# Optimization experiments

Hardware: AMD Instinct MI355X
Metric: run time of the kernel (lower is better)

The kernel has to match this reference:

```python
import jax, jax.numpy as jnp
import numpy as np

N = 100000      # nodes
E = 600000      # edges per relation (avg degree 6 per relation here per edge list)
R = 3           # num_relations
D_IN = 128
D_OUT = 128


def setup_inputs() -> dict:
    key = jax.random.key(0)
    ks = jax.random.split(key, 7)
    x = jax.random.normal(ks[0], (N, D_IN), dtype=jnp.float32)
    src = jax.random.randint(ks[1], (R, E), 0, N, dtype=jnp.int32)   # column indices of sparse adj
    dst = jax.random.randint(ks[2], (R, E), 0, N, dtype=jnp.int32)   # row indices of sparse adj
    vals = jax.random.uniform(ks[3], (R, E), dtype=jnp.float32)      # nonzero values
    scale = 1.0 / np.sqrt(D_IN)
    W_self = jax.random.normal(ks[4], (D_OUT, D_IN), dtype=jnp.float32) * scale
    b_self = jnp.zeros((D_OUT,), dtype=jnp.float32)
    W_rels = jax.random.normal(ks[5], (R, D_OUT, D_IN), dtype=jnp.float32) * scale
    return {"x": x, "src": src, "dst": dst, "vals": vals,
            "W_self": W_self, "b_self": b_self, "W_rels": W_rels}


def reference(x, src, dst, vals, W_self, b_self, W_rels):
    # self-loop: Linear(in_dim, out_dim) with bias
    out = x @ W_self.T + b_self                               # [N, D_OUT]
    n = x.shape[0]
    for r in range(R):
        # sparse.mm(adj_r, x): row i gets sum_j adj[i,j] * x[j]
        msg = vals[r][:, None] * x[src[r]]                    # [E, D_IN] gather
        agg = jax.ops.segment_sum(msg, dst[r], num_segments=n)  # [N, D_IN] scatter-add
        out = out + agg @ W_rels[r].T                         # per-relation Linear (no bias)
    return out
```

## Files before the change

kernel.cpp:

```cpp
#include <hip/hip_runtime.h>


typedef __attribute__((ext_vector_type(8))) short bf16x8;
typedef __attribute__((ext_vector_type(4))) float f32x4;
typedef unsigned short u16;

__device__ inline void split2(float v, u16& h, u16& l) {
  unsigned u = __float_as_uint(v);
  u16 hu = (u16)(u >> 16);
  float r = v - __uint_as_float((unsigned)hu << 16);
  unsigned ur = __float_as_uint(r);
  l = (u16)((ur + 0x7FFF + ((ur >> 16) & 1)) >> 16);
  h = hu;
}


__global__ void hist_kernel(const int* __restrict__ dst, int* __restrict__ cursor,
                            int total, int N, int E) {
  int i = blockIdx.x * 256 + threadIdx.x;
  if (i >= total) return;
  int r = i / E;
  atomicAdd(&cursor[r * N + dst[i]], 1);
}

__global__ __launch_bounds__(256)
void scanA_kernel(const int* __restrict__ cursor, int* __restrict__ blockSums, int keys) {
  int t = threadIdx.x;
  int idx = blockIdx.x * 1024 + t * 4;
  int s = 0;
  if (idx < keys) {
    int4 v = *(const int4*)(cursor + idx);
    s = v.x + v.y + v.z + v.w;
  }
  __shared__ int lds[256];
  lds[t] = s;
  __syncthreads();
  for (int off = 128; off > 0; off >>= 1) {
    if (t < off) lds[t] += lds[t + off];
    __syncthreads();
  }
  if (t == 0) blockSums[blockIdx.x] = lds[0];
}

__global__ __launch_bounds__(1024)
void scanB_kernel(int* __restrict__ blockSums, int nb) {
  __shared__ int lds[1024];
  int t = threadIdx.x;
  int v0 = (t < nb) ? blockSums[t] : 0;
  lds[t] = v0;
  __syncthreads();
  for (int off = 1; off < 1024; off <<= 1) {
    int v = (t >= off) ? lds[t - off] : 0;
    __syncthreads();
    lds[t] += v;
    __syncthreads();
  }
  if (t < nb) blockSums[t] = lds[t] - v0;
}

__global__ __launch_bounds__(256)
void scanC_kernel(int* __restrict__ cursor, const int* __restrict__ blockSums, int keys) {
  int t = threadIdx.x;
  int idx = blockIdx.x * 1024 + t * 4;
  int4 v = make_int4(0, 0, 0, 0);
  if (idx < keys) v = *(const int4*)(cursor + idx);
  int s = v.x + v.y + v.z + v.w;
  __shared__ int lds[256];
  lds[t] = s;
  __syncthreads();
  for (int off = 1; off < 256; off <<= 1) {
    int u = (t >= off) ? lds[t - off] : 0;
    __syncthreads();
    lds[t] += u;
    __syncthreads();
  }
  int run = blockSums[blockIdx.x] + lds[t] - s;
  if (idx < keys) {
    int4 o;
    o.x = run;              run += v.x;
    o.y = run;              run += v.y;
    o.z = run;              run += v.z;
    o.w = run;
    *(int4*)(cursor + idx) = o;
  }
}

__global__ void fill_kernel(const int* __restrict__ dst, const int* __restrict__ src,
                            const float* __restrict__ vals, int* __restrict__ cursor,
                            int2* __restrict__ edges, int total, int N, int E) {
  int i = blockIdx.x * 256 + threadIdx.x;
  if (i >= total) return;
  int r = i / E;
  int key = r * N + dst[i];
  int p = atomicAdd(&cursor[key], 1);
  edges[p] = make_int2(src[i], __float_as_int(vals[i]));
}


__global__ __launch_bounds__(256)
void aggregate_kernel(const float* __restrict__ x, const int2* __restrict__ edges,
                      const int* __restrict__ cursor, float* __restrict__ Agg,
                      int N, int R, int keys) {
  int wid = blockIdx.x * 4 + (threadIdx.x >> 6);
  if (wid >= keys) return;
  int lane = threadIdx.x & 63;
  int r = (wid < N) ? 0 : ((wid < 2 * N) ? 1 : 2);
  int d = wid - r * N;
  int pstart = (wid == 0) ? 0 : cursor[wid - 1];
  int pend   = cursor[wid];
  float2 acc = {0.f, 0.f};
  int p = pstart;
  for (; p + 4 <= pend; p += 4) {
    int2 e0 = edges[p + 0];
    int2 e1 = edges[p + 1];
    int2 e2 = edges[p + 2];
    int2 e3 = edges[p + 3];
    float2 x0 = *(const float2*)(x + (size_t)e0.x * 128 + lane * 2);
    float2 x1 = *(const float2*)(x + (size_t)e1.x * 128 + lane * 2);
    float2 x2 = *(const float2*)(x + (size_t)e2.x * 128 + lane * 2);
    float2 x3 = *(const float2*)(x + (size_t)e3.x * 128 + lane * 2);
    float v0 = __int_as_float(e0.y), v1 = __int_as_float(e1.y);
    float v2 = __int_as_float(e2.y), v3 = __int_as_float(e3.y);
    acc.x += v0 * x0.x; acc.y += v0 * x0.y;
    acc.x += v1 * x1.x; acc.y += v1 * x1.y;
    acc.x += v2 * x2.x; acc.y += v2 * x2.y;
    acc.x += v3 * x3.x; acc.y += v3 * x3.y;
  }
  for (; p < pend; ++p) {
    int2 e = edges[p];
    float2 xv = *(const float2*)(x + (size_t)e.x * 128 + lane * 2);
    float v = __int_as_float(e.y);
    acc.x += v * xv.x; acc.y += v * xv.y;
  }
  *(float2*)(Agg + (size_t)d * (R * 128) + r * 128 + lane * 2) = acc;
}


__global__ __launch_bounds__(256)
void split_w_kernel(const float* __restrict__ Wself, const float* __restrict__ Wrels,
                    u16* __restrict__ Whi, u16* __restrict__ Wlo) {
  int e = (blockIdx.x * 256 + threadIdx.x) * 4;
  if (e >= 128 * 512) return;
  int n = e >> 9;
  int k = e & 511;
  #pragma unroll
  for (int j = 0; j < 4; ++j) {
    int kk = k + j;
    float v;
    if (kk < 128) v = Wself[n * 128 + kk];
    else {
      int q = (kk - 128) >> 7;
      v = Wrels[q * 16384 + n * 128 + ((kk - 128) & 127)];
    }
    u16 h, l;
    split2(v, h, l);
    Whi[n * 512 + kk] = h;
    Wlo[n * 512 + kk] = l;
  }
}


__global__ __launch_bounds__(256)
void gemm_mfma(const float* __restrict__ x, const float* __restrict__ Agg,
               const u16* __restrict__ Whi, const u16* __restrict__ Wlo,
               const float* __restrict__ bias, float* __restrict__ out, int N) {
  __shared__ __align__(16) u16 Ah[128][40];
  __shared__ __align__(16) u16 Al[128][40];
  __shared__ __align__(16) u16 Bh[128][40];
  __shared__ __align__(16) u16 Bl[128][40];

  const int m0   = blockIdx.x * 128;
  const int t    = threadIdx.x;
  const int lane = t & 63;
  const int wave = t >> 6;
  const int wm   = wave >> 1;
  const int wn   = wave & 1;
  const int lr   = lane & 15;
  const int kg   = lane >> 4;

  f32x4 acc[4][4];
  #pragma unroll
  for (int i = 0; i < 4; ++i)
    #pragma unroll
    for (int j = 0; j < 4; ++j)
      #pragma unroll
      for (int c = 0; c < 4; ++c) acc[i][j][c] = 0.f;

  for (int ph = 0; ph < 16; ++ph) {
    __syncthreads();
    #pragma unroll
    for (int i = 0; i < 4; ++i) {
      int L   = t + i * 256;
      int row = L >> 3;
      int c4  = L & 7;
      int gm  = m0 + row;
      float4 v = make_float4(0.f, 0.f, 0.f, 0.f);
      if (gm < N) {
        const float* Ap = (ph < 4) ? (x + (size_t)gm * 128 + ph * 32)
                                   : (Agg + (size_t)gm * 384 + (ph - 4) * 32);
        v = *(const float4*)(Ap + c4 * 4);
      }
      ushort4 h4, l4;
      split2(v.x, h4.x, l4.x);
      split2(v.y, h4.y, l4.y);
      split2(v.z, h4.z, l4.z);
      split2(v.w, h4.w, l4.w);
      *(ushort4*)&Ah[row][c4 * 4] = h4;
      *(ushort4*)&Al[row][c4 * 4] = l4;
    }
    #pragma unroll
    for (int i = 0; i < 4; ++i) {
      int L   = t + i * 256;
      int row = L >> 3;
      int c4  = L & 7;
      *(ushort4*)&Bh[row][c4 * 4] = *(const ushort4*)(Whi + row * 512 + ph * 32 + c4 * 4);
      *(ushort4*)&Bl[row][c4 * 4] = *(const ushort4*)(Wlo + row * 512 + ph * 32 + c4 * 4);
    }
    __syncthreads();

    bf16x8 ah[4], al[4], bh[4], bl[4];
    #pragma unroll
    for (int i = 0; i < 4; ++i) {
      ah[i] = *(const bf16x8*)&Ah[wm * 64 + i * 16 + lr][kg * 8];
      al[i] = *(const bf16x8*)&Al[wm * 64 + i * 16 + lr][kg * 8];
      bh[i] = *(const bf16x8*)&Bh[wn * 64 + i * 16 + lr][kg * 8];
      bl[i] = *(const bf16x8*)&Bl[wn * 64 + i * 16 + lr][kg * 8];
    }
    #pragma unroll
    for (int i = 0; i < 4; ++i)
      #pragma unroll
      for (int j = 0; j < 4; ++j) {
        acc[i][j] = __builtin_amdgcn_mfma_f32_16x16x32_bf16(ah[i], bh[j], acc[i][j], 0, 0, 0);
        acc[i][j] = __builtin_amdgcn_mfma_f32_16x16x32_bf16(al[i], bh[j], acc[i][j], 0, 0, 0);
        acc[i][j] = __builtin_amdgcn_mfma_f32_16x16x32_bf16(ah[i], bl[j], acc[i][j], 0, 0, 0);
      }
  }

  float bv[4];
  #pragma unroll
  for (int j = 0; j < 4; ++j) bv[j] = bias[wn * 64 + j * 16 + lr];
  #pragma unroll
  for (int i = 0; i < 4; ++i) {
    #pragma unroll
    for (int j = 0; j < 4; ++j) {
      int col = wn * 64 + j * 16 + lr;
      #pragma unroll
      for (int rg = 0; rg < 4; ++rg) {
        int gm = m0 + wm * 64 + i * 16 + kg * 4 + rg;
        if (gm < N) out[(size_t)gm * 128 + col] = acc[i][j][rg] + bv[j];
      }
    }
  }
}


__global__ __launch_bounds__(256, 4)
void gemm_kernel(const float* __restrict__ x, const float* __restrict__ Wself,
                 const float* __restrict__ Wrels, const float* __restrict__ bias,
                 float* __restrict__ out, float* __restrict__ Y, int N, int R) {
  __shared__ float xs[64][68];
  __shared__ float ws[64][68];
  const int m0 = blockIdx.x * 64;
  const int nt = blockIdx.y;
  const float* Wp = (nt < 2) ? (Wself + nt * 64 * 128)
                             : (Wrels + (size_t)(nt - 2) * 64 * 128);
  const int t  = threadIdx.x;
  const int tm = t >> 4;
  const int tn = t & 15;
  float acc[4][4] = {};
  for (int ph = 0; ph < 2; ++ph) {
    __syncthreads();
    #pragma unroll
    for (int i = 0; i < 4; ++i) {
      int L = t + i * 256;
      int row = L >> 4;
      int c4 = L & 15;
      int gm = m0 + row;
      float4 xv = make_float4(0.f, 0.f, 0.f, 0.f);
      if (gm < N) xv = ((const float4*)(x + (size_t)gm * 128 + ph * 64))[c4];
      *((float4*)&xs[row][c4 * 4]) = xv;
      float4 wv = ((const float4*)(Wp + (size_t)row * 128 + ph * 64))[c4];
      *((float4*)&ws[row][c4 * 4]) = wv;
    }
    __syncthreads();
    #pragma unroll
    for (int kk = 0; kk < 16; ++kk) {
      float4 a[4], b[4];
      #pragma unroll
      for (int i = 0; i < 4; ++i) a[i] = *(const float4*)&xs[i * 16 + tm][kk * 4];
      #pragma unroll
      for (int j = 0; j < 4; ++j) b[j] = *(const float4*)&ws[j * 16 + tn][kk * 4];
      #pragma unroll
      for (int i = 0; i < 4; ++i)
        #pragma unroll
        for (int j = 0; j < 4; ++j) {
          acc[i][j] += a[i].x * b[j].x;
          acc[i][j] += a[i].y * b[j].y;
          acc[i][j] += a[i].z * b[j].z;
          acc[i][j] += a[i].w * b[j].w;
        }
    }
  }
  const int YS = R * 128;
  #pragma unroll
  for (int i = 0; i < 4; ++i) {
    int gm = m0 + i * 16 + tm;
    if (gm >= N) continue;
    #pragma unroll
    for (int j = 0; j < 4; ++j) {
      int col = j * 16 + tn;
      float v = acc[i][j];
      if (nt < 2) {
        int oc = nt * 64 + col;
        out[(size_t)gm * 128 + oc] = v + bias[oc];
      } else {
        int q = nt - 2;
        Y[(size_t)gm * YS + q * 64 + col] = v;
      }
    }
  }
}

__global__ __launch_bounds__(256)
void scatter_kernel(const float* __restrict__ Y, const int* __restrict__ src,
                    const int* __restrict__ dst, const float* __restrict__ vals,
                    float* __restrict__ out, long long total_slots, int E, int YS4) {
  long long tid = (long long)blockIdx.x * 256 + threadIdx.x;
  long long slot = tid >> 5;
  int lane = (int)(tid & 31);
  if (slot >= total_slots) return;
  int r = (int)(slot / E);
  int s = src[slot];
  int d = dst[slot];
  float v = vals[slot];
  float4 y = ((const float4*)Y)[(size_t)s * YS4 + r * 32 + lane];
  float* o = out + (size_t)d * 128 + lane * 4;
  atomicAdd(o + 0, v * y.x);
  atomicAdd(o + 1, v * y.y);
  atomicAdd(o + 2, v * y.z);
  atomicAdd(o + 3, v * y.w);
}


extern "C" void kernel_launch(void* const* d_in, const int* in_sizes, int n_in,
                              void* d_out, int out_size, void* d_ws, size_t ws_size,
                              hipStream_t stream) {
  const float* x     = (const float*)d_in[0];
  const int*   src   = (const int*)d_in[1];
  const int*   dst   = (const int*)d_in[2];
  const float* vals  = (const float*)d_in[3];
  const float* Wself = (const float*)d_in[4];
  const float* bias  = (const float*)d_in[5];
  const float* Wrels = (const float*)d_in[6];
  float*       out   = (float*)d_out;

  const int N = in_sizes[0] / 128;
  const int R = in_sizes[6] / (128 * 128);
  const int E = in_sizes[1] / R;
  const int total = R * E;
  const int keys = R * N;
  const int nb = (keys + 1023) / 1024;

  size_t aggBytes  = (size_t)N * R * 128 * sizeof(float);
  size_t curBytes  = ((size_t)keys * sizeof(int) + 255) & ~(size_t)255;
  size_t edgeBytes = ((size_t)total * sizeof(int2) + 255) & ~(size_t)255;
  size_t bsBytes   = ((size_t)nb * sizeof(int) + 255) & ~(size_t)255;
  size_t wBytes    = ((size_t)128 * 512 * sizeof(u16) + 255) & ~(size_t)255;
  size_t need = aggBytes + curBytes + edgeBytes + bsBytes + 2 * wBytes + 512;

  if (ws_size >= need && R == 3 && nb <= 1024 && (keys % 4) == 0) {
    char* base = (char*)d_ws;
    float* Agg       = (float*)base;  base += aggBytes;
    int*   cursor    = (int*)base;    base += curBytes;
    int*   blockSums = (int*)base;    base += bsBytes;
    int2*  edges     = (int2*)base;   base += edgeBytes;
    u16*   Whi       = (u16*)base;    base += wBytes;
    u16*   Wlo       = (u16*)base;

    hipMemsetAsync(cursor, 0, (size_t)keys * sizeof(int), stream);
    hist_kernel<<<(total + 255) / 256, 256, 0, stream>>>(dst, cursor, total, N, E);
    scanA_kernel<<<nb, 256, 0, stream>>>(cursor, blockSums, keys);
    scanB_kernel<<<1, 1024, 0, stream>>>(blockSums, nb);
    scanC_kernel<<<nb, 256, 0, stream>>>(cursor, blockSums, keys);
    fill_kernel<<<(total + 255) / 256, 256, 0, stream>>>(dst, src, vals, cursor, edges, total, N, E);
    split_w_kernel<<<64, 256, 0, stream>>>(Wself, Wrels, Whi, Wlo);
    aggregate_kernel<<<(keys + 3) / 4, 256, 0, stream>>>(x, edges, cursor, Agg, N, R, keys);
    gemm_mfma<<<(N + 127) / 128, 256, 0, stream>>>(x, Agg, Whi, Wlo, bias, out, N);
  } else {
    float* Y = (float*)d_ws;
    dim3 g1((N + 63) / 64, 2 + 2 * R);
    gemm_kernel<<<g1, 256, 0, stream>>>(x, Wself, Wrels, bias, out, Y, N, R);
    long long slots = (long long)R * E;
    long long threads = slots * 32;
    int blocks = (int)((threads + 255) / 256);
    scatter_kernel<<<blocks, 256, 0, stream>>>(Y, src, dst, vals, out, slots, E, R * 32);
  }
}
```

Baseline: 557.4 us.

## Store aggregated features as bf16 hi/lo and load GEMM tiles via direct-to-LDS

The aggregation kernel now splits each wave into two half-waves that process alternating edges with float4 loads, reduces them with a shuffle, and writes the result pre-split into bf16 hi and lo arrays instead of fp32. The GEMM then streams the pre-split Agg and W tiles straight into LDS with global_load_lds using an XOR-swizzled layout and a doubled K step per phase. Only the x part is still split on the fly. This removes the fp32 Agg round trip and the per-element split work in the GEMM, at the cost of a second Agg buffer and a more intricate swizzle.

```diff
diff --git a/kernel.cpp b/kernel.cpp
--- a/kernel.cpp
+++ b/kernel.cpp
@@ -12,6 +12,12 @@
   unsigned ur = __float_as_uint(r);
   l = (u16)((ur + 0x7FFF + ((ur >> 16) & 1)) >> 16);
   h = hu;
+}
+
+__device__ inline void gload_lds16(const void* g, void* lds) {
+  __builtin_amdgcn_global_load_lds(
+      (const __attribute__((address_space(1))) unsigned*)g,
+      (__attribute__((address_space(3))) unsigned*)lds, 16, 0, 0);
 }
 
 
@@ -99,40 +105,53 @@
 
 __global__ __launch_bounds__(256)
 void aggregate_kernel(const float* __restrict__ x, const int2* __restrict__ edges,
-                      const int* __restrict__ cursor, float* __restrict__ Agg,
-                      int N, int R, int keys) {
+                      const int* __restrict__ cursor, u16* __restrict__ Agghi,
+                      u16* __restrict__ Agglo, int N, int keys) {
   int wid = blockIdx.x * 4 + (threadIdx.x >> 6);
   if (wid >= keys) return;
-  int lane = threadIdx.x & 63;
+  int lane    = threadIdx.x & 63;
+  int lane_in = lane & 31;
+  int sub     = lane >> 5;
   int r = (wid < N) ? 0 : ((wid < 2 * N) ? 1 : 2);
   int d = wid - r * N;
   int pstart = (wid == 0) ? 0 : cursor[wid - 1];
   int pend   = cursor[wid];
-  float2 acc = {0.f, 0.f};
-  int p = pstart;
-  for (; p + 4 <= pend; p += 4) {
+  float4 acc = make_float4(0.f, 0.f, 0.f, 0.f);
+  int p = pstart + sub;
+  for (; p + 6 < pend; p += 8) {
     int2 e0 = edges[p + 0];
-    int2 e1 = edges[p + 1];
-    int2 e2 = edges[p + 2];
-    int2 e3 = edges[p + 3];
-    float2 x0 = *(const float2*)(x + (size_t)e0.x * 128 + lane * 2);
-    float2 x1 = *(const float2*)(x + (size_t)e1.x * 128 + lane * 2);
-    float2 x2 = *(const float2*)(x + (size_t)e2.x * 128 + lane * 2);
-    float2 x3 = *(const float2*)(x + (size_t)e3.x * 128 + lane * 2);
+    int2 e1 = edges[p + 2];
+    int2 e2 = edges[p + 4];
+    int2 e3 = edges[p + 6];
+    float4 x0 = *(const float4*)(x + (size_t)e0.x * 128 + lane_in * 4);
+    float4 x1 = *(const float4*)(x + (size_t)e1.x * 128 + lane_in * 4);
+    float4 x2 = *(const float4*)(x + (size_t)e2.x * 128 + lane_in * 4);
+    float4 x3 = *(const float4*)(x + (size_t)e3.x * 128 + lane_in * 4);
     float v0 = __int_as_float(e0.y), v1 = __int_as_float(e1.y);
     float v2 = __int_as_float(e2.y), v3 = __int_as_float(e3.y);
-    acc.x += v0 * x0.x; acc.y += v0 * x0.y;
-    acc.x += v1 * x1.x; acc.y += v1 * x1.y;
-    acc.x += v2 * x2.x; acc.y += v2 * x2.y;
-    acc.x += v3 * x3.x; acc.y += v3 * x3.y;
-  }
-  for (; p < pend; ++p) {
+    acc.x += v0 * x0.x; acc.y += v0 * x0.y; acc.z += v0 * x0.z; acc.w += v0 * x0.w;
+    acc.x += v1 * x1.x; acc.y += v1 * x1.y; acc.z += v1 * x1.z; acc.w += v1 * x1.w;
+    acc.x += v2 * x2.x; acc.y += v2 * x2.y; acc.z += v2 * x2.z; acc.w += v2 * x2.w;
+    acc.x += v3 * x3.x; acc.y += v3 * x3.y; acc.z += v3 * x3.z; acc.w += v3 * x3.w;
+  }
+  for (; p < pend; p += 2) {
     int2 e = edges[p];
-    float2 xv = *(const float2*)(x + (size_t)e.x * 128 + lane * 2);
+    float4 xv = *(const float4*)(x + (size_t)e.x * 128 + lane_in * 4);
     float v = __int_as_float(e.y);
-    acc.x += v * xv.x; acc.y += v * xv.y;
-  }
-  *(float2*)(Agg + (size_t)d * (R * 128) + r * 128 + lane * 2) = acc;
+    acc.x += v * xv.x; acc.y += v * xv.y; acc.z += v * xv.z; acc.w += v * xv.w;
+  }
+  acc.x += __shfl_xor(acc.x, 32);
+  acc.y += __shfl_xor(acc.y, 32);
+  acc.z += __shfl_xor(acc.z, 32);
+  acc.w += __shfl_xor(acc.w, 32);
+  u16 h0, l0, h1, l1, h2, l2, h3, l3;
+  split2(acc.x, h0, l0); split2(acc.y, h1, l1);
+  split2(acc.z, h2, l2); split2(acc.w, h3, l3);
+  ushort4 w4;
+  if (sub) { w4.x = l0; w4.y = l1; w4.z = l2; w4.w = l3; }
+  else     { w4.x = h0; w4.y = h1; w4.z = h2; w4.w = h3; }
+  u16* dstp = (sub ? Agglo : Agghi) + (size_t)d * 384 + r * 128 + lane_in * 4;
+  *(ushort4*)dstp = w4;
 }
 
 
@@ -161,13 +180,14 @@
 
 
 __global__ __launch_bounds__(256)
-void gemm_mfma(const float* __restrict__ x, const float* __restrict__ Agg,
-               const u16* __restrict__ Whi, const u16* __restrict__ Wlo,
-               const float* __restrict__ bias, float* __restrict__ out, int N) {
-  __shared__ __align__(16) u16 Ah[128][40];
-  __shared__ __align__(16) u16 Al[128][40];
-  __shared__ __align__(16) u16 Bh[128][40];
-  __shared__ __align__(16) u16 Bl[128][40];
+void gemm_mfma(const float* __restrict__ x, const u16* __restrict__ Agghi,
+               const u16* __restrict__ Agglo, const u16* __restrict__ Whi,
+               const u16* __restrict__ Wlo, const float* __restrict__ bias,
+               float* __restrict__ out, int N) {
+  __shared__ __align__(16) u16 Ah[128 * 64];
+  __shared__ __align__(16) u16 Al[128 * 64];
+  __shared__ __align__(16) u16 Bh[128 * 64];
+  __shared__ __align__(16) u16 Bl[128 * 64];
 
   const int m0   = blockIdx.x * 128;
   const int t    = threadIdx.x;
@@ -186,54 +206,88 @@
       #pragma unroll
       for (int c = 0; c < 4; ++c) acc[i][j][c] = 0.f;
 
-  for (int ph = 0; ph < 16; ++ph) {
-    __syncthreads();
+  for (int ph = 0; ph < 8; ++ph) {
+    __syncthreads();
+
+    #pragma unroll
+    for (int j = 0; j < 8; ++j) {
+      int p    = wave * 8 + j;
+      int tile = p >> 4;
+      int rg   = p & 15;
+      int row  = rg * 8 + (lane >> 3);
+      int c16  = (lane & 7) ^ (row & 7);
+      const u16* gsrc = (tile ? Wlo : Whi) + row * 512 + ph * 64 + c16 * 8;
+      u16* ldst = (tile ? Bl : Bh) + rg * 512 + lane * 8;
+      gload_lds16(gsrc, ldst);
+    }
+    if (ph >= 2) {
+      int kofs = ph * 64 - 128;
+      #pragma unroll
+      for (int j = 0; j < 8; ++j) {
+        int p    = wave * 8 + j;
+        int tile = p >> 4;
+        int rg   = p & 15;
+        int row  = rg * 8 + (lane >> 3);
+        int grow = m0 + row; if (grow > N - 1) grow = N - 1;
+        int c16  = (lane & 7) ^ (row & 7);
+        const u16* gsrc = (tile ? Agglo : Agghi) + (size_t)grow * 384 + kofs + c16 * 8;
+        u16* ldst = (tile ? Al : Ah) + rg * 512 + lane * 8;
+        gload_lds16(gsrc, ldst);
+      }
+    } else {
+      #pragma unroll
+      for (int i = 0; i < 4; ++i) {
+        int q   = t + i * 256;
+        int row = q >> 3;
+        int c16 = q & 7;
+        int gm  = m0 + row;
+        float4 va = make_float4(0.f, 0.f, 0.f, 0.f);
+        float4 vb = make_float4(0.f, 0.f, 0.f, 0.f);
+        if (gm < N) {
+          const float* xp = x + (size_t)gm * 128 + ph * 64 + c16 * 8;
+          va = *(const float4*)xp;
+          vb = *(const float4*)(xp + 4);
+        }
+        ushort4 ha, la, hb, lb;
+        split2(va.x, ha.x, la.x); split2(va.y, ha.y, la.y);
+        split2(va.z, ha.z, la.z); split2(va.w, ha.w, la.w);
+        split2(vb.x, hb.x, lb.x); split2(vb.y, hb.y, lb.y);
+        split2(vb.z, hb.z, lb.z); split2(vb.w, hb.w, lb.w);
+        int slot = c16 ^ (row & 7);
+        int idx = row * 64 + slot * 8;
+        *(ushort4*)&Ah[idx]     = ha;
+        *(ushort4*)&Ah[idx + 4] = hb;
+        *(ushort4*)&Al[idx]     = la;
+        *(ushort4*)&Al[idx + 4] = lb;
+      }
+    }
+    __syncthreads();
+
+    bf16x8 ah[4][2], al[4][2], bh[4][2], bl[4][2];
     #pragma unroll
     for (int i = 0; i < 4; ++i) {
-      int L   = t + i * 256;
-      int row = L >> 3;
-      int c4  = L & 7;
-      int gm  = m0 + row;
-      float4 v = make_float4(0.f, 0.f, 0.f, 0.f);
-      if (gm < N) {
-        const float* Ap = (ph < 4) ? (x + (size_t)gm * 128 + ph * 32)
-                                   : (Agg + (size_t)gm * 384 + (ph - 4) * 32);
-        v = *(const float4*)(Ap + c4 * 4);
+      int arow = wm * 64 + i * 16 + lr;
+      int brow = wn * 64 + i * 16 + lr;
+      #pragma unroll
+      for (int ks = 0; ks < 2; ++ks) {
+        int ac = ((ks * 4 + kg) ^ (arow & 7)) * 8;
+        int bc = ((ks * 4 + kg) ^ (brow & 7)) * 8;
+        ah[i][ks] = *(const bf16x8*)&Ah[arow * 64 + ac];
+        al[i][ks] = *(const bf16x8*)&Al[arow * 64 + ac];
+        bh[i][ks] = *(const bf16x8*)&Bh[brow * 64 + bc];
+        bl[i][ks] = *(const bf16x8*)&Bl[brow * 64 + bc];
       }
-      ushort4 h4, l4;
-      split2(v.x, h4.x, l4.x);
-      split2(v.y, h4.y, l4.y);
-      split2(v.z, h4.z, l4.z);
-      split2(v.w, h4.w, l4.w);
-      *(ushort4*)&Ah[row][c4 * 4] = h4;
-      *(ushort4*)&Al[row][c4 * 4] = l4;
-    }
-    #pragma unroll
-    for (int i = 0; i < 4; ++i) {
-      int L   = t + i * 256;
-      int row = L >> 3;
-      int c4  = L & 7;
-      *(ushort4*)&Bh[row][c4 * 4] = *(const ushort4*)(Whi + row * 512 + ph * 32 + c4 * 4);
-      *(ushort4*)&Bl[row][c4 * 4] = *(const ushort4*)(Wlo + row * 512 + ph * 32 + c4 * 4);
-    }
-    __syncthreads();
-
-    bf16x8 ah[4], al[4], bh[4], bl[4];
-    #pragma unroll
-    for (int i = 0; i < 4; ++i) {
-      ah[i] = *(const bf16x8*)&Ah[wm * 64 + i * 16 + lr][kg * 8];
-      al[i] = *(const bf16x8*)&Al[wm * 64 + i * 16 + lr][kg * 8];
-      bh[i] = *(const bf16x8*)&Bh[wn * 64 + i * 16 + lr][kg * 8];
-      bl[i] = *(const bf16x8*)&Bl[wn * 64 + i * 16 + lr][kg * 8];
     }
     #pragma unroll
     for (int i = 0; i < 4; ++i)
       #pragma unroll
-      for (int j = 0; j < 4; ++j) {
-        acc[i][j] = __builtin_amdgcn_mfma_f32_16x16x32_bf16(ah[i], bh[j], acc[i][j], 0, 0, 0);
-        acc[i][j] = __builtin_amdgcn_mfma_f32_16x16x32_bf16(al[i], bh[j], acc[i][j], 0, 0, 0);
-        acc[i][j] = __builtin_amdgcn_mfma_f32_16x16x32_bf16(ah[i], bl[j], acc[i][j], 0, 0, 0);
-      }
+      for (int j = 0; j < 4; ++j)
+        #pragma unroll
+        for (int ks = 0; ks < 2; ++ks) {
+          acc[i][j] = __builtin_amdgcn_mfma_f32_16x16x32_bf16(ah[i][ks], bh[j][ks], acc[i][j], 0, 0, 0);
+          acc[i][j] = __builtin_amdgcn_mfma_f32_16x16x32_bf16(al[i][ks], bh[j][ks], acc[i][j], 0, 0, 0);
+          acc[i][j] = __builtin_amdgcn_mfma_f32_16x16x32_bf16(ah[i][ks], bl[j][ks], acc[i][j], 0, 0, 0);
+        }
   }
 
   float bv[4];
@@ -361,16 +415,17 @@
   const int keys = R * N;
   const int nb = (keys + 1023) / 1024;
 
-  size_t aggBytes  = (size_t)N * R * 128 * sizeof(float);
+  size_t aggBytes  = (((size_t)N * R * 128 * sizeof(u16)) + 255) & ~(size_t)255;
   size_t curBytes  = ((size_t)keys * sizeof(int) + 255) & ~(size_t)255;
   size_t edgeBytes = ((size_t)total * sizeof(int2) + 255) & ~(size_t)255;
   size_t bsBytes   = ((size_t)nb * sizeof(int) + 255) & ~(size_t)255;
   size_t wBytes    = ((size_t)128 * 512 * sizeof(u16) + 255) & ~(size_t)255;
-  size_t need = aggBytes + curBytes + edgeBytes + bsBytes + 2 * wBytes + 512;
+  size_t need = 2 * aggBytes + curBytes + edgeBytes + bsBytes + 2 * wBytes + 512;
 
   if (ws_size >= need && R == 3 && nb <= 1024 && (keys % 4) == 0) {
     char* base = (char*)d_ws;
-    float* Agg       = (float*)base;  base += aggBytes;
+    u16*   Agghi     = (u16*)base;    base += aggBytes;
+    u16*   Agglo     = (u16*)base;    base += aggBytes;
     int*   cursor    = (int*)base;    base += curBytes;
     int*   blockSums = (int*)base;    base += bsBytes;
     int2*  edges     = (int2*)base;   base += edgeBytes;
@@ -384,8 +439,8 @@
     scanC_kernel<<<nb, 256, 0, stream>>>(cursor, blockSums, keys);
     fill_kernel<<<(total + 255) / 256, 256, 0, stream>>>(dst, src, vals, cursor, edges, total, N, E);
     split_w_kernel<<<64, 256, 0, stream>>>(Wself, Wrels, Whi, Wlo);
-    aggregate_kernel<<<(keys + 3) / 4, 256, 0, stream>>>(x, edges, cursor, Agg, N, R, keys);
-    gemm_mfma<<<(N + 127) / 128, 256, 0, stream>>>(x, Agg, Whi, Wlo, bias, out, N);
+    aggregate_kernel<<<(keys + 3) / 4, 256, 0, stream>>>(x, edges, cursor, Agghi, Agglo, N, keys);
+    gemm_mfma<<<(N + 127) / 128, 256, 0, stream>>>(x, Agghi, Agglo, Whi, Wlo, bias, out, N);
   } else {
     float* Y = (float*)d_ws;
     dim3 g1((N + 63) / 64, 2 + 2 * R);
```

Result: faster. 537.2 us (-3.6%).
